# Performance work log

Hardware: AMD Instinct MI355X
Metric: run time of the kernel (lower is better)

## Reference

```python
import jax, jax.numpy as jnp
import numpy as np

BETA = 0.25  # commitment_beta


def setup_inputs() -> dict:
    key = jax.random.key(0)
    k1, k2 = jax.random.split(key)
    B, S, D, K = 4, 2048, 256, 8192
    z_e = jax.random.normal(k1, (B, S, D), dtype=jnp.float32)
    # codebook init ~ uniform(-1/K, 1/K) in the original; scale is irrelevant for correctness,
    # use normal scaled similarly small.
    codebook = jax.random.uniform(k2, (K, D), dtype=jnp.float32, minval=-1.0 / K, maxval=1.0 / K)
    return {"z_e": z_e, "codebook": codebook}


def reference(z_e, codebook):
    B, S, D = z_e.shape
    flat = z_e.reshape(-1, D)  # [N, D], N = B*S
    distances = (
        jnp.sum(flat * flat, axis=1, keepdims=True)
        - 2.0 * (flat @ codebook.T)
        + jnp.sum(codebook * codebook, axis=1)[None, :]
    )
    indices = jnp.argmin(distances, axis=1)  # [N]
    z_q = codebook[indices].reshape(B, S, D)
    codebook_loss = jnp.mean((jax.lax.stop_gradient(z_e) - z_q) ** 2)
    commitment_loss = jnp.mean((z_e - jax.lax.stop_gradient(z_q)) ** 2)
    vq_loss = codebook_loss + BETA * commitment_loss
    # straight-through estimator
    z_q_st = z_e + jax.lax.stop_gradient(z_q - z_e)
    return z_q_st, indices.reshape(B, S), vq_loss
```

## Files before the change

kernel.cpp:

```cpp
#include <hip/hip_runtime.h>
#include <stdint.h>

#define N_ROWS  8192
#define DIM     256
#define K_CODES 8192
#define SPLITK  8
#define KS      1024
#define ROWS_B  64
#define KT_CODES 256
#define LSLOTS  32
#define GSLOTS  8
#define MARGIN_ACC 1.0e-4f

typedef unsigned long long u64;
typedef unsigned short u16;
typedef short s16x8 __attribute__((ext_vector_type(8)));
typedef float f32x4 __attribute__((ext_vector_type(4)));

__device__ __forceinline__ u64 u64min(u64 a, u64 b) { return a < b ? a : b; }

__device__ __forceinline__ u16 f2bf(float f) {
    unsigned u = __float_as_uint(f);
    u += 0x7fffu + ((u >> 16) & 1u);
    return (u16)(u >> 16);
}

__device__ __forceinline__ unsigned fkey(float f) {
    unsigned b = __float_as_uint(f);
    return (b & 0x80000000u) ? ~b : (b | 0x80000000u);
}
__device__ __forceinline__ float funkey(unsigned k) {
    unsigned b = (k & 0x80000000u) ? (k ^ 0x80000000u) : ~k;
    return __uint_as_float(b);
}

__device__ __forceinline__ void gld16(void* lds, const void* g) {
    __builtin_amdgcn_global_load_lds(
        (const __attribute__((address_space(1))) unsigned int*)g,
        (__attribute__((address_space(3))) unsigned int*)lds, 16, 0, 0);
}

__device__ __forceinline__ float exact_dot(const float* __restrict__ xr,
                                           const float* __restrict__ cr) {
    const float4* x4 = (const float4*)xr;
    const float4* c4 = (const float4*)cr;
    float acc = 0.0f;
#pragma unroll 8
    for (int c = 0; c < DIM / 4; c++) {
        float4 xv = x4[c], cv = c4[c];
        acc = __builtin_fmaf(xv.x, cv.x, acc);
        acc = __builtin_fmaf(xv.y, cv.y, acc);
        acc = __builtin_fmaf(xv.z, cv.z, acc);
        acc = __builtin_fmaf(xv.w, cv.w, acc);
    }
    return acc;
}

__global__ __launch_bounds__(256) void vq_prep(const float* __restrict__ z_e,
                                               const float* __restrict__ cb,
                                               u16* __restrict__ zb,
                                               u16* __restrict__ cbb,
                                               float* __restrict__ xnorm,
                                               float* __restrict__ cnorm) {
    int wid  = (blockIdx.x * 256 + threadIdx.x) >> 6;
    int lane = threadIdx.x & 63;
    const float* src; u16* d16; float* dn;
    if (wid < N_ROWS) { src = z_e + (size_t)wid * DIM; d16 = zb + (size_t)wid * DIM; dn = xnorm + wid; }
    else              { int k = wid - N_ROWS;
                        src = cb  + (size_t)k   * DIM; d16 = cbb + (size_t)k * DIM; dn = cnorm + k; }
    float4 v = *(const float4*)(src + lane * 4);
    ushort4 h;
    h.x = f2bf(v.x); h.y = f2bf(v.y); h.z = f2bf(v.z); h.w = f2bf(v.w);
    *(ushort4*)(d16 + lane * 4) = h;
    float s = (v.x * v.x + v.y * v.y) + (v.z * v.z + v.w * v.w);
#pragma unroll
    for (int off = 1; off < 64; off <<= 1)
        s += __shfl_xor(s, off, 64);
    if (lane == 0) *dn = s;
}

__global__ __launch_bounds__(256, 3) void vq_mfma(const u16* __restrict__ zb,
                                                  const u16* __restrict__ cbb,
                                                  int* __restrict__ cand_cnt,
                                                  u64* __restrict__ candkey) {
    __shared__ u16      Xs[ROWS_B * DIM];
    __shared__ float    lcd[ROWS_B * LSLOTS];
    __shared__ int      lci[ROWS_B * LSLOTS];
    __shared__ int      lcnt[ROWS_B];
    __shared__ unsigned smax[ROWS_B];

    const int tid   = threadIdx.x;
    const int lane  = tid & 63;
    const int wave  = tid >> 6;
    const int quad  = lane >> 4;
    const int l16   = lane & 15;
    const int split = blockIdx.x;
    const int n0    = blockIdx.y * ROWS_B;

    if (tid < ROWS_B) { lcnt[tid] = 0; smax[tid] = 0u; }

#pragma unroll
    for (int t = 0; t < 8; t++) {
        int ubase = wave * 512 + t * 64;
        int u     = ubase + lane;
        int row   = u >> 5;
        int p     = u & 31;
        int csrc  = p ^ (row & 7);
        gld16(&Xs[ubase * 8], zb + (size_t)(n0 + row) * DIM + csrc * 8);
    }
    __syncthreads();

    for (int kt = 0; kt < KS / KT_CODES; kt++) {
        const int kw = split * KS + kt * KT_CODES + wave * 64;
        f32x4 acc[4][4];
#pragma unroll
        for (int i = 0; i < 4; i++)
#pragma unroll
            for (int j = 0; j < 4; j++)
#pragma unroll
                for (int e = 0; e < 4; e++) acc[i][j][e] = 0.0f;

#pragma unroll
        for (int ks = 0; ks < 8; ks++) {
            s16x8 af[4], bfr[4];
#pragma unroll
            for (int i = 0; i < 4; i++)
                af[i] = *(const s16x8*)&Xs[(i * 16 + l16) * DIM +
                                           (((ks << 2) | quad) ^ (l16 & 7)) * 8];
#pragma unroll
            for (int j = 0; j < 4; j++)
                bfr[j] = *(const s16x8*)(cbb + (size_t)(kw + j * 16 + l16) * DIM +
                                         ks * 32 + quad * 8);
#pragma unroll
            for (int i = 0; i < 4; i++)
#pragma unroll
                for (int j = 0; j < 4; j++)
                    acc[i][j] = __builtin_amdgcn_mfma_f32_16x16x32_bf16(af[i], bfr[j], acc[i][j], 0, 0, 0);
        }

#pragma unroll
        for (int i = 0; i < 4; i++)
#pragma unroll
            for (int r = 0; r < 4; r++) {
                int rl = i * 16 + quad * 4 + r;
                float m = fmaxf(fmaxf(acc[i][0][r], acc[i][1][r]),
                                fmaxf(acc[i][2][r], acc[i][3][r]));
                m = fmaxf(m, __shfl_xor(m, 1, 64));
                m = fmaxf(m, __shfl_xor(m, 2, 64));
                m = fmaxf(m, __shfl_xor(m, 4, 64));
                m = fmaxf(m, __shfl_xor(m, 8, 64));
                if (l16 == 0) atomicMax(&smax[rl], fkey(m));
                float g   = funkey(smax[rl]);
                float thr = fmaxf(g, m) - MARGIN_ACC;
                float mj = fmaxf(fmaxf(acc[i][0][r], acc[i][1][r]),
                                 fmaxf(acc[i][2][r], acc[i][3][r]));
                if (mj >= thr) {
#pragma unroll
                    for (int j = 0; j < 4; j++) {
                        float d = acc[i][j][r];
                        if (d >= thr) {
                            int pos = atomicAdd(&lcnt[rl], 1);
                            if (pos < LSLOTS) {
                                lcd[rl * LSLOTS + pos] = d;
                                lci[rl * LSLOTS + pos] = kw + j * 16 + l16;
                            }
                        }
                    }
                }
            }
    }

    __syncthreads();

    if (tid < ROWS_B) {
        int   row  = tid, n = n0 + row;
        int   raw  = lcnt[row];
        int   cnt  = raw < LSLOTS ? raw : LSLOTS;
        float thr  = funkey(smax[row]) - MARGIN_ACC;
        int   base = (n * SPLITK + split) * GSLOTS;
        int   w = 0, kept = 0;
        for (int s = 0; s < cnt; s++) {
            if (lcd[row * LSLOTS + s] >= thr) {
                kept++;
                if (w < GSLOTS) {
                    float d = lcd[row * LSLOTS + s];
                    candkey[base + w] = ((u64)__float_as_uint(d) << 32)
                                        | (unsigned)lci[row * LSLOTS + s];
                    w++;
                }
            }
        }
        cand_cnt[n * SPLITK + split] = (raw > LSLOTS || kept > GSLOTS) ? -1 : w;
    }
}

__global__ __launch_bounds__(256) void vq_finalize(const float* __restrict__ z_e,
                                                   const float* __restrict__ cb,
                                                   const float* __restrict__ xnorm,
                                                   const float* __restrict__ cnorm,
                                                   const int* __restrict__ cand_cnt,
                                                   const u64* __restrict__ candkey,
                                                   float* __restrict__ out_zq,
                                                   float* __restrict__ out_idx,
                                                   float* __restrict__ rowloss) {
    const int n    = blockIdx.x * 4 + (threadIdx.x >> 6);
    const int lane = threadIdx.x & 63;
    const int s    = lane >> 3;
    const int t    = lane & 7;

    const float* xr = z_e + (size_t)n * DIM;
    const float  xn = xnorm[n];

    int  cnt   = cand_cnt[n * SPLITK + s];
    u64  ck    = candkey[(size_t)n * 64 + lane];
    bool valid = (cnt >= 0) && (t < cnt);
    float dot  = valid ? __uint_as_float((unsigned)(ck >> 32)) : -3.0e38f;

    float gmax = dot;
#pragma unroll
    for (int off = 1; off < 64; off <<= 1)
        gmax = fmaxf(gmax, __shfl_xor(gmax, off, 64));
    float thr = gmax - MARGIN_ACC;

    u64 key = ~0ULL;
    if (valid && dot >= thr) {
        int  idx   = (int)(unsigned)(ck & 0xffffffffu);
        float m    = exact_dot(xr, cb + (size_t)idx * DIM);
        float dist = __builtin_fmaf(-2.0f, m, xn) + cnorm[idx];
        key = ((u64)__float_as_uint(dist) << 32) | (unsigned)idx;
    }

#pragma unroll
    for (int fs = 0; fs < SPLITK; fs++) {
        if (__builtin_expect(cand_cnt[n * SPLITK + fs] < 0, 0)) {
            for (int it = 0; it < KS / 64; it++) {
                int k = fs * KS + it * 64 + lane;
                float m    = exact_dot(xr, cb + (size_t)k * DIM);
                float dist = __builtin_fmaf(-2.0f, m, xn) + cnorm[k];
                key = u64min(key, ((u64)__float_as_uint(dist) << 32) | (unsigned)k);
            }
        }
    }

#pragma unroll
    for (int off = 1; off < 64; off <<= 1)
        key = u64min(key, __shfl_xor(key, off, 64));

    int idx = (int)(unsigned)(key & 0xffffffffu);
    if (key == ~0ULL) idx = 0;

    float4 x = *(const float4*)(xr + lane * 4);
    float4 c = *(const float4*)(cb + (size_t)idx * DIM + lane * 4);
    float4 st;
    st.x = x.x + (c.x - x.x); st.y = x.y + (c.y - x.y);
    st.z = x.z + (c.z - x.z); st.w = x.w + (c.w - x.w);
    *(float4*)(out_zq + (size_t)n * DIM + lane * 4) = st;

    float d0 = x.x - c.x, d1 = x.y - c.y, d2 = x.z - c.z, d3 = x.w - c.w;
    float s2 = (d0 * d0 + d1 * d1) + (d2 * d2 + d3 * d3);
#pragma unroll
    for (int off = 1; off < 64; off <<= 1)
        s2 += __shfl_xor(s2, off, 64);
    if (lane == 0) {
        rowloss[n] = s2;
        out_idx[n] = (float)idx;
    }
}

__global__ __launch_bounds__(256) void vq_loss(const float* __restrict__ rowloss,
                                               float* __restrict__ out_loss) {
    __shared__ double sd[256];
    double s = 0.0;
    for (int i = threadIdx.x; i < N_ROWS; i += 256) s += (double)rowloss[i];
    sd[threadIdx.x] = s;
    __syncthreads();
    for (int off = 128; off; off >>= 1) {
        if (threadIdx.x < off) sd[threadIdx.x] += sd[threadIdx.x + off];
        __syncthreads();
    }
    if (threadIdx.x == 0) {
        double mean = sd[0] / (double)((size_t)N_ROWS * DIM);
        out_loss[0] = (float)(1.25 * mean);
    }
}

extern "C" void kernel_launch(void* const* d_in, const int* in_sizes, int n_in,
                              void* d_out, int out_size, void* d_ws, size_t ws_size,
                              hipStream_t stream) {
    const float* z_e = (const float*)d_in[0];
    const float* cb  = (const float*)d_in[1];

    float* out   = (float*)d_out;
    float* zq    = out;
    float* oidx  = out + (size_t)N_ROWS * DIM;
    float* oloss = oidx + N_ROWS;

    u16*   zb       = (u16*)d_ws;
    u16*   cbb      = zb + (size_t)N_ROWS * DIM;
    float* xnorm    = (float*)(cbb + (size_t)K_CODES * DIM);
    float* cnorm    = xnorm + N_ROWS;
    float* rowloss  = cnorm + K_CODES;
    int*   cand_cnt = (int*)(rowloss + N_ROWS);
    u64*   candkey  = (u64*)(cand_cnt + N_ROWS * SPLITK);

    vq_prep    <<<(N_ROWS + K_CODES) / 4, 256, 0, stream>>>(z_e, cb, zb, cbb, xnorm, cnorm);
    vq_mfma    <<<dim3(SPLITK, N_ROWS / ROWS_B), 256, 0, stream>>>(zb, cbb, cand_cnt, candkey);
    vq_finalize<<<N_ROWS / 4, 256, 0, stream>>>(z_e, cb, xnorm, cnorm, cand_cnt, candkey, zq, oidx, rowloss);
    vq_loss    <<<1, 256, 0, stream>>>(rowloss, oloss);
}
```

Measured before the change: 200.9 us.

## Prefetch codebook fragments into registers and replace loss reduction with atomics

The MFMA kernel now loads all 32 B-fragments for a K-tile into registers before the MFMA loop, with a sched_barrier to keep the loads grouped ahead of compute. Launch bounds occupancy drops from 3 to 2 waves to make room for the extra registers. The row-loss buffer and its block-reduction kernel are replaced by a double atomicAdd per row in finalize, plus a tiny final kernel. The double accumulator is zeroed in prep. The trade-off is lower occupancy and atomic contention in exchange for more memory-level parallelism and less reduction work.

```diff
diff --git a/kernel.cpp b/kernel.cpp
--- a/kernel.cpp
+++ b/kernel.cpp
@@ -61,7 +61,9 @@
                                                u16* __restrict__ zb,
                                                u16* __restrict__ cbb,
                                                float* __restrict__ xnorm,
-                                               float* __restrict__ cnorm) {
+                                               float* __restrict__ cnorm,
+                                               double* __restrict__ dacc) {
+    if (blockIdx.x == 0 && threadIdx.x == 0) *dacc = 0.0;
     int wid  = (blockIdx.x * 256 + threadIdx.x) >> 6;
     int lane = threadIdx.x & 63;
     const float* src; u16* d16; float* dn;
@@ -79,7 +81,7 @@
     if (lane == 0) *dn = s;
 }
 
-__global__ __launch_bounds__(256, 3) void vq_mfma(const u16* __restrict__ zb,
+__global__ __launch_bounds__(256, 2) void vq_mfma(const u16* __restrict__ zb,
                                                   const u16* __restrict__ cbb,
                                                   int* __restrict__ cand_cnt,
                                                   u64* __restrict__ candkey) {
@@ -112,6 +114,16 @@
 
     for (int kt = 0; kt < KS / KT_CODES; kt++) {
         const int kw = split * KS + kt * KT_CODES + wave * 64;
+        const u16* bbase = cbb + (size_t)(kw + l16) * DIM + quad * 8;
+
+        s16x8 bb[32];
+#pragma unroll
+        for (int ks = 0; ks < 8; ks++)
+#pragma unroll
+            for (int j = 0; j < 4; j++)
+                bb[j * 8 + ks] = *(const s16x8*)(bbase + (size_t)(j * 16) * DIM + ks * 32);
+        __builtin_amdgcn_sched_barrier(0);
+
         f32x4 acc[4][4];
 #pragma unroll
         for (int i = 0; i < 4; i++)
@@ -122,20 +134,16 @@
 
 #pragma unroll
         for (int ks = 0; ks < 8; ks++) {
-            s16x8 af[4], bfr[4];
+            s16x8 af[4];
 #pragma unroll
             for (int i = 0; i < 4; i++)
                 af[i] = *(const s16x8*)&Xs[(i * 16 + l16) * DIM +
                                            (((ks << 2) | quad) ^ (l16 & 7)) * 8];
 #pragma unroll
-            for (int j = 0; j < 4; j++)
-                bfr[j] = *(const s16x8*)(cbb + (size_t)(kw + j * 16 + l16) * DIM +
-                                         ks * 32 + quad * 8);
-#pragma unroll
             for (int i = 0; i < 4; i++)
 #pragma unroll
                 for (int j = 0; j < 4; j++)
-                    acc[i][j] = __builtin_amdgcn_mfma_f32_16x16x32_bf16(af[i], bfr[j], acc[i][j], 0, 0, 0);
+                    acc[i][j] = __builtin_amdgcn_mfma_f32_16x16x32_bf16(af[i], bb[j * 8 + ks], acc[i][j], 0, 0, 0);
         }
 
 #pragma unroll
@@ -202,7 +210,7 @@
                                                    const u64* __restrict__ candkey,
                                                    float* __restrict__ out_zq,
                                                    float* __restrict__ out_idx,
-                                                   float* __restrict__ rowloss) {
+                                                   double* __restrict__ dacc) {
     const int n    = blockIdx.x * 4 + (threadIdx.x >> 6);
     const int lane = threadIdx.x & 63;
     const int s    = lane >> 3;
@@ -262,26 +270,15 @@
     for (int off = 1; off < 64; off <<= 1)
         s2 += __shfl_xor(s2, off, 64);
     if (lane == 0) {
-        rowloss[n] = s2;
         out_idx[n] = (float)idx;
-    }
-}
-
-__global__ __launch_bounds__(256) void vq_loss(const float* __restrict__ rowloss,
-                                               float* __restrict__ out_loss) {
-    __shared__ double sd[256];
-    double s = 0.0;
-    for (int i = threadIdx.x; i < N_ROWS; i += 256) s += (double)rowloss[i];
-    sd[threadIdx.x] = s;
-    __syncthreads();
-    for (int off = 128; off; off >>= 1) {
-        if (threadIdx.x < off) sd[threadIdx.x] += sd[threadIdx.x + off];
-        __syncthreads();
-    }
-    if (threadIdx.x == 0) {
-        double mean = sd[0] / (double)((size_t)N_ROWS * DIM);
-        out_loss[0] = (float)(1.25 * mean);
-    }
+        atomicAdd(dacc, (double)s2);
+    }
+}
+
+__global__ void vq_loss_final(const double* __restrict__ dacc,
+                              float* __restrict__ out_loss) {
+    if (threadIdx.x == 0)
+        out_loss[0] = (float)(1.25 * (*dacc) / (double)((size_t)N_ROWS * DIM));
 }
 
 extern "C" void kernel_launch(void* const* d_in, const int* in_sizes, int n_in,
@@ -295,16 +292,16 @@
     float* oidx  = out + (size_t)N_ROWS * DIM;
     float* oloss = oidx + N_ROWS;
 
-    u16*   zb       = (u16*)d_ws;
-    u16*   cbb      = zb + (size_t)N_ROWS * DIM;
-    float* xnorm    = (float*)(cbb + (size_t)K_CODES * DIM);
-    float* cnorm    = xnorm + N_ROWS;
-    float* rowloss  = cnorm + K_CODES;
-    int*   cand_cnt = (int*)(rowloss + N_ROWS);
-    u64*   candkey  = (u64*)(cand_cnt + N_ROWS * SPLITK);
-
-    vq_prep    <<<(N_ROWS + K_CODES) / 4, 256, 0, stream>>>(z_e, cb, zb, cbb, xnorm, cnorm);
-    vq_mfma    <<<dim3(SPLITK, N_ROWS / ROWS_B), 256, 0, stream>>>(zb, cbb, cand_cnt, candkey);
-    vq_finalize<<<N_ROWS / 4, 256, 0, stream>>>(z_e, cb, xnorm, cnorm, cand_cnt, candkey, zq, oidx, rowloss);
-    vq_loss    <<<1, 256, 0, stream>>>(rowloss, oloss);
-}
+    u16*    zb       = (u16*)d_ws;
+    u16*    cbb      = zb + (size_t)N_ROWS * DIM;
+    float*  xnorm    = (float*)(cbb + (size_t)K_CODES * DIM);
+    float*  cnorm    = xnorm + N_ROWS;
+    double* dacc     = (double*)(cnorm + K_CODES);
+    int*    cand_cnt = (int*)(dacc + 1);
+    u64*    candkey  = (u64*)(cand_cnt + N_ROWS * SPLITK);
+
+    vq_prep      <<<(N_ROWS + K_CODES) / 4, 256, 0, stream>>>(z_e, cb, zb, cbb, xnorm, cnorm, dacc);
+    vq_mfma      <<<dim3(SPLITK, N_ROWS / ROWS_B), 256, 0, stream>>>(zb, cbb, cand_cnt, candkey);
+    vq_finalize  <<<N_ROWS / 4, 256, 0, stream>>>(z_e, cb, xnorm, cnorm, cand_cnt, candkey, zq, oidx, dacc);
+    vq_loss_final<<<1, 64, 0, stream>>>(dacc, oloss);
+}
```

New measurement: 277.7 us. +38.2%, slower.

## Double split-K factor and split finalize into pick and apply kernels

Applied to the files above, without the earlier changes.

Raises the codebook split from 8 to 16 chunks of 512 codes, doubling the MFMA grid so more workgroups run in parallel. The finalize step now handles 128 candidate slots per row, two per lane, and is split into a pick kernel that writes the chosen index and a separate apply kernel that writes z_q, the index and the row loss. This adds an extra kernel launch, an extra index buffer round trip, more candidate traffic and more exact re-ranking dot products per row.

```diff
diff --git a/kernel.cpp b/kernel.cpp
--- a/kernel.cpp
+++ b/kernel.cpp
@@ -4,8 +4,8 @@
 #define N_ROWS  8192
 #define DIM     256
 #define K_CODES 8192
-#define SPLITK  8
-#define KS      1024
+#define SPLITK  16
+#define KS      512
 #define ROWS_B  64
 #define KT_CODES 256
 #define LSLOTS  32
@@ -194,43 +194,50 @@
     }
 }
 
-__global__ __launch_bounds__(256) void vq_finalize(const float* __restrict__ z_e,
-                                                   const float* __restrict__ cb,
-                                                   const float* __restrict__ xnorm,
-                                                   const float* __restrict__ cnorm,
-                                                   const int* __restrict__ cand_cnt,
-                                                   const u64* __restrict__ candkey,
-                                                   float* __restrict__ out_zq,
-                                                   float* __restrict__ out_idx,
-                                                   float* __restrict__ rowloss) {
+__global__ __launch_bounds__(256) void vq_pick(const float* __restrict__ z_e,
+                                               const float* __restrict__ cb,
+                                               const float* __restrict__ xnorm,
+                                               const float* __restrict__ cnorm,
+                                               const int* __restrict__ cand_cnt,
+                                               const u64* __restrict__ candkey,
+                                               int* __restrict__ idx_out) {
     const int n    = blockIdx.x * 4 + (threadIdx.x >> 6);
     const int lane = threadIdx.x & 63;
-    const int s    = lane >> 3;
-    const int t    = lane & 7;
 
     const float* xr = z_e + (size_t)n * DIM;
     const float  xn = xnorm[n];
 
-    int  cnt   = cand_cnt[n * SPLITK + s];
-    u64  ck    = candkey[(size_t)n * 64 + lane];
-    bool valid = (cnt >= 0) && (t < cnt);
-    float dot  = valid ? __uint_as_float((unsigned)(ck >> 32)) : -3.0e38f;
-
-    float gmax = dot;
+    u64  ck[2];
+    bool valid[2];
+    float dot[2];
+#pragma unroll
+    for (int h = 0; h < 2; h++) {
+        int slot = h * 64 + lane;
+        int s    = slot >> 3;
+        int t    = slot & 7;
+        int cnt  = cand_cnt[n * SPLITK + s];
+        ck[h]    = candkey[(size_t)n * (SPLITK * GSLOTS) + slot];
+        valid[h] = (cnt >= 0) && (t < cnt);
+        dot[h]   = valid[h] ? __uint_as_float((unsigned)(ck[h] >> 32)) : -3.0e38f;
+    }
+
+    float gmax = fmaxf(dot[0], dot[1]);
 #pragma unroll
     for (int off = 1; off < 64; off <<= 1)
         gmax = fmaxf(gmax, __shfl_xor(gmax, off, 64));
     float thr = gmax - MARGIN_ACC;
 
     u64 key = ~0ULL;
-    if (valid && dot >= thr) {
-        int  idx   = (int)(unsigned)(ck & 0xffffffffu);
-        float m    = exact_dot(xr, cb + (size_t)idx * DIM);
-        float dist = __builtin_fmaf(-2.0f, m, xn) + cnorm[idx];
-        key = ((u64)__float_as_uint(dist) << 32) | (unsigned)idx;
-    }
-
-#pragma unroll
+#pragma unroll
+    for (int h = 0; h < 2; h++) {
+        if (valid[h] && dot[h] >= thr) {
+            int  idx   = (int)(unsigned)(ck[h] & 0xffffffffu);
+            float m    = exact_dot(xr, cb + (size_t)idx * DIM);
+            float dist = __builtin_fmaf(-2.0f, m, xn) + cnorm[idx];
+            key = u64min(key, ((u64)__float_as_uint(dist) << 32) | (unsigned)idx);
+        }
+    }
+
     for (int fs = 0; fs < SPLITK; fs++) {
         if (__builtin_expect(cand_cnt[n * SPLITK + fs] < 0, 0)) {
             for (int it = 0; it < KS / 64; it++) {
@@ -246,10 +253,24 @@
     for (int off = 1; off < 64; off <<= 1)
         key = u64min(key, __shfl_xor(key, off, 64));
 
-    int idx = (int)(unsigned)(key & 0xffffffffu);
-    if (key == ~0ULL) idx = 0;
-
-    float4 x = *(const float4*)(xr + lane * 4);
+    if (lane == 0) {
+        int idx = (int)(unsigned)(key & 0xffffffffu);
+        if (key == ~0ULL) idx = 0;
+        idx_out[n] = idx;
+    }
+}
+
+__global__ __launch_bounds__(64) void vq_apply(const float* __restrict__ z_e,
+                                               const float* __restrict__ cb,
+                                               const int* __restrict__ idx_in,
+                                               float* __restrict__ out_zq,
+                                               float* __restrict__ out_idx,
+                                               float* __restrict__ rowloss) {
+    int n    = blockIdx.x;
+    int lane = threadIdx.x;
+    int idx  = idx_in[n];
+
+    float4 x = *(const float4*)(z_e + (size_t)n * DIM + lane * 4);
     float4 c = *(const float4*)(cb + (size_t)idx * DIM + lane * 4);
     float4 st;
     st.x = x.x + (c.x - x.x); st.y = x.y + (c.y - x.y);
@@ -300,11 +321,13 @@
     float* xnorm    = (float*)(cbb + (size_t)K_CODES * DIM);
     float* cnorm    = xnorm + N_ROWS;
     float* rowloss  = cnorm + K_CODES;
-    int*   cand_cnt = (int*)(rowloss + N_ROWS);
+    int*   idxw     = (int*)(rowloss + N_ROWS);
+    int*   cand_cnt = idxw + N_ROWS;
     u64*   candkey  = (u64*)(cand_cnt + N_ROWS * SPLITK);
 
-    vq_prep    <<<(N_ROWS + K_CODES) / 4, 256, 0, stream>>>(z_e, cb, zb, cbb, xnorm, cnorm);
-    vq_mfma    <<<dim3(SPLITK, N_ROWS / ROWS_B), 256, 0, stream>>>(zb, cbb, cand_cnt, candkey);
-    vq_finalize<<<N_ROWS / 4, 256, 0, stream>>>(z_e, cb, xnorm, cnorm, cand_cnt, candkey, zq, oidx, rowloss);
-    vq_loss    <<<1, 256, 0, stream>>>(rowloss, oloss);
-}
+    vq_prep <<<(N_ROWS + K_CODES) / 4, 256, 0, stream>>>(z_e, cb, zb, cbb, xnorm, cnorm);
+    vq_mfma <<<dim3(SPLITK, N_ROWS / ROWS_B), 256, 0, stream>>>(zb, cbb, cand_cnt, candkey);
+    vq_pick <<<N_ROWS / 4, 256, 0, stream>>>(z_e, cb, xnorm, cnorm, cand_cnt, candkey, idxw);
+    vq_apply<<<N_ROWS, 64, 0, stream>>>(z_e, cb, idxw, zq, oidx, rowloss);
+    vq_loss <<<1, 256, 0, stream>>>(rowloss, oloss);
+}
```

Measured after the change: 234.3 us. +16.6%, slower.

## Double split-K, shrink candidate slots, and restage exact rescoring through LDS

Applied to the files above, without the earlier changes.

Splits the codebook search across 16 slices of 512 codes instead of 8 of 1024, lowers per-row local candidate slots, and raises the occupancy hint of the MFMA kernel to 4 blocks. The finalize kernel becomes one 64-thread block per row that gathers threshold-passing candidates into shared memory and rescores them in fp32 from LDS-staged codebook rows, instead of each lane doing a strided global dot product. The loss reduction now uses a 1024-thread block. The aim is more parallelism in the search and cheaper candidate rescoring, at the cost of twice as many candidate entries to merge and a higher chance of slot overflow falling back to brute-force slices.

```diff
diff --git a/kernel.cpp b/kernel.cpp
--- a/kernel.cpp
+++ b/kernel.cpp
@@ -4,12 +4,13 @@
 #define N_ROWS  8192
 #define DIM     256
 #define K_CODES 8192
-#define SPLITK  8
-#define KS      1024
+#define SPLITK  16
+#define KS      512
 #define ROWS_B  64
 #define KT_CODES 256
-#define LSLOTS  32
+#define LSLOTS  12
 #define GSLOTS  8
+#define MAXS    16
 #define MARGIN_ACC 1.0e-4f
 
 typedef unsigned long long u64;
@@ -40,8 +41,8 @@
         (__attribute__((address_space(3))) unsigned int*)lds, 16, 0, 0);
 }
 
-__device__ __forceinline__ float exact_dot(const float* __restrict__ xr,
-                                           const float* __restrict__ cr) {
+__device__ __forceinline__ float exact_dot_g(const float* __restrict__ xr,
+                                             const float* __restrict__ cr) {
     const float4* x4 = (const float4*)xr;
     const float4* c4 = (const float4*)cr;
     float acc = 0.0f;
@@ -79,7 +80,7 @@
     if (lane == 0) *dn = s;
 }
 
-__global__ __launch_bounds__(256, 3) void vq_mfma(const u16* __restrict__ zb,
+__global__ __launch_bounds__(256, 4) void vq_mfma(const u16* __restrict__ zb,
                                                   const u16* __restrict__ cbb,
                                                   int* __restrict__ cand_cnt,
                                                   u64* __restrict__ candkey) {
@@ -194,48 +195,96 @@
     }
 }
 
-__global__ __launch_bounds__(256) void vq_finalize(const float* __restrict__ z_e,
-                                                   const float* __restrict__ cb,
-                                                   const float* __restrict__ xnorm,
-                                                   const float* __restrict__ cnorm,
-                                                   const int* __restrict__ cand_cnt,
-                                                   const u64* __restrict__ candkey,
-                                                   float* __restrict__ out_zq,
-                                                   float* __restrict__ out_idx,
-                                                   float* __restrict__ rowloss) {
-    const int n    = blockIdx.x * 4 + (threadIdx.x >> 6);
-    const int lane = threadIdx.x & 63;
-    const int s    = lane >> 3;
-    const int t    = lane & 7;
+__global__ __launch_bounds__(64) void vq_pick_apply(const float* __restrict__ z_e,
+                                                    const float* __restrict__ cb,
+                                                    const float* __restrict__ xnorm,
+                                                    const float* __restrict__ cnorm,
+                                                    const int* __restrict__ cand_cnt,
+                                                    const u64* __restrict__ candkey,
+                                                    float* __restrict__ out_zq,
+                                                    float* __restrict__ out_idx,
+                                                    float* __restrict__ rowloss) {
+    __shared__ float xs[DIM];
+    __shared__ float cs[4][DIM + 4];
+    __shared__ int   sidx[MAXS];
+    __shared__ int   scnt;
+
+    const int n    = blockIdx.x;
+    const int lane = threadIdx.x;
+    if (lane == 0) scnt = 0;
 
     const float* xr = z_e + (size_t)n * DIM;
     const float  xn = xnorm[n];
-
-    int  cnt   = cand_cnt[n * SPLITK + s];
-    u64  ck    = candkey[(size_t)n * 64 + lane];
-    bool valid = (cnt >= 0) && (t < cnt);
-    float dot  = valid ? __uint_as_float((unsigned)(ck >> 32)) : -3.0e38f;
-
-    float gmax = dot;
+    float4 x = *(const float4*)(xr + lane * 4);
+    *(float4*)&xs[lane * 4] = x;
+
+    u64  ck0 = candkey[(size_t)n * (SPLITK * GSLOTS) + lane];
+    u64  ck1 = candkey[(size_t)n * (SPLITK * GSLOTS) + 64 + lane];
+    int  c0  = cand_cnt[n * SPLITK + (lane >> 3)];
+    int  c1  = cand_cnt[n * SPLITK + 8 + (lane >> 3)];
+    bool v0  = (c0 >= 0) && ((lane & 7) < c0);
+    bool v1  = (c1 >= 0) && ((lane & 7) < c1);
+    float d0 = v0 ? __uint_as_float((unsigned)(ck0 >> 32)) : -3.0e38f;
+    float d1 = v1 ? __uint_as_float((unsigned)(ck1 >> 32)) : -3.0e38f;
+
+    float gmax = fmaxf(d0, d1);
 #pragma unroll
     for (int off = 1; off < 64; off <<= 1)
         gmax = fmaxf(gmax, __shfl_xor(gmax, off, 64));
     float thr = gmax - MARGIN_ACC;
 
     u64 key = ~0ULL;
-    if (valid && dot >= thr) {
-        int  idx   = (int)(unsigned)(ck & 0xffffffffu);
-        float m    = exact_dot(xr, cb + (size_t)idx * DIM);
-        float dist = __builtin_fmaf(-2.0f, m, xn) + cnorm[idx];
-        key = ((u64)__float_as_uint(dist) << 32) | (unsigned)idx;
-    }
-
-#pragma unroll
+    if (v0 && d0 >= thr) {
+        int p = atomicAdd(&scnt, 1);
+        int idx = (int)(unsigned)(ck0 & 0xffffffffu);
+        if (p < MAXS) sidx[p] = idx;
+        else {
+            float m = exact_dot_g(xr, cb + (size_t)idx * DIM);
+            float dist = __builtin_fmaf(-2.0f, m, xn) + cnorm[idx];
+            key = u64min(key, ((u64)__float_as_uint(dist) << 32) | (unsigned)idx);
+        }
+    }
+    if (v1 && d1 >= thr) {
+        int p = atomicAdd(&scnt, 1);
+        int idx = (int)(unsigned)(ck1 & 0xffffffffu);
+        if (p < MAXS) sidx[p] = idx;
+        else {
+            float m = exact_dot_g(xr, cb + (size_t)idx * DIM);
+            float dist = __builtin_fmaf(-2.0f, m, xn) + cnorm[idx];
+            key = u64min(key, ((u64)__float_as_uint(dist) << 32) | (unsigned)idx);
+        }
+    }
+    __syncthreads();
+
+    int sc = scnt; if (sc > MAXS) sc = MAXS;
+    for (int b = 0; b < sc; b += 4) {
+        int take = sc - b; if (take > 4) take = 4;
+        int g   = lane >> 4;
+        int l16 = lane & 15;
+        if (g < take) {
+            const float* cr = cb + (size_t)sidx[b + g] * DIM;
+#pragma unroll
+            for (int p = 0; p < 4; p++)
+                *(float4*)&cs[g][p * 64 + l16 * 4] = *(const float4*)(cr + p * 64 + l16 * 4);
+        }
+        __syncthreads();
+        if (lane < take) {
+            int idx = sidx[b + lane];
+            float acc = 0.0f;
+#pragma unroll 8
+            for (int d = 0; d < DIM; d++)
+                acc = __builtin_fmaf(xs[d], cs[lane][d], acc);
+            float dist = __builtin_fmaf(-2.0f, acc, xn) + cnorm[idx];
+            key = u64min(key, ((u64)__float_as_uint(dist) << 32) | (unsigned)idx);
+        }
+        __syncthreads();
+    }
+
     for (int fs = 0; fs < SPLITK; fs++) {
         if (__builtin_expect(cand_cnt[n * SPLITK + fs] < 0, 0)) {
             for (int it = 0; it < KS / 64; it++) {
                 int k = fs * KS + it * 64 + lane;
-                float m    = exact_dot(xr, cb + (size_t)k * DIM);
+                float m    = exact_dot_g(xr, cb + (size_t)k * DIM);
                 float dist = __builtin_fmaf(-2.0f, m, xn) + cnorm[k];
                 key = u64min(key, ((u64)__float_as_uint(dist) << 32) | (unsigned)k);
             }
@@ -249,15 +298,14 @@
     int idx = (int)(unsigned)(key & 0xffffffffu);
     if (key == ~0ULL) idx = 0;
 
-    float4 x = *(const float4*)(xr + lane * 4);
     float4 c = *(const float4*)(cb + (size_t)idx * DIM + lane * 4);
     float4 st;
     st.x = x.x + (c.x - x.x); st.y = x.y + (c.y - x.y);
     st.z = x.z + (c.z - x.z); st.w = x.w + (c.w - x.w);
     *(float4*)(out_zq + (size_t)n * DIM + lane * 4) = st;
 
-    float d0 = x.x - c.x, d1 = x.y - c.y, d2 = x.z - c.z, d3 = x.w - c.w;
-    float s2 = (d0 * d0 + d1 * d1) + (d2 * d2 + d3 * d3);
+    float e0 = x.x - c.x, e1 = x.y - c.y, e2 = x.z - c.z, e3 = x.w - c.w;
+    float s2 = (e0 * e0 + e1 * e1) + (e2 * e2 + e3 * e3);
 #pragma unroll
     for (int off = 1; off < 64; off <<= 1)
         s2 += __shfl_xor(s2, off, 64);
@@ -267,14 +315,14 @@
     }
 }
 
-__global__ __launch_bounds__(256) void vq_loss(const float* __restrict__ rowloss,
-                                               float* __restrict__ out_loss) {
-    __shared__ double sd[256];
+__global__ __launch_bounds__(1024) void vq_loss(const float* __restrict__ rowloss,
+                                                float* __restrict__ out_loss) {
+    __shared__ double sd[1024];
     double s = 0.0;
-    for (int i = threadIdx.x; i < N_ROWS; i += 256) s += (double)rowloss[i];
+    for (int i = threadIdx.x; i < N_ROWS; i += 1024) s += (double)rowloss[i];
     sd[threadIdx.x] = s;
     __syncthreads();
-    for (int off = 128; off; off >>= 1) {
+    for (int off = 512; off; off >>= 1) {
         if (threadIdx.x < off) sd[threadIdx.x] += sd[threadIdx.x + off];
         __syncthreads();
     }
@@ -303,8 +351,8 @@
     int*   cand_cnt = (int*)(rowloss + N_ROWS);
     u64*   candkey  = (u64*)(cand_cnt + N_ROWS * SPLITK);
 
-    vq_prep    <<<(N_ROWS + K_CODES) / 4, 256, 0, stream>>>(z_e, cb, zb, cbb, xnorm, cnorm);
-    vq_mfma    <<<dim3(SPLITK, N_ROWS / ROWS_B), 256, 0, stream>>>(zb, cbb, cand_cnt, candkey);
-    vq_finalize<<<N_ROWS / 4, 256, 0, stream>>>(z_e, cb, xnorm, cnorm, cand_cnt, candkey, zq, oidx, rowloss);
-    vq_loss    <<<1, 256, 0, stream>>>(rowloss, oloss);
-}
+    vq_prep      <<<(N_ROWS + K_CODES) / 4, 256, 0, stream>>>(z_e, cb, zb, cbb, xnorm, cnorm);
+    vq_mfma      <<<dim3(SPLITK, N_ROWS / ROWS_B), 256, 0, stream>>>(zb, cbb, cand_cnt, candkey);
+    vq_pick_apply<<<N_ROWS, 64, 0, stream>>>(z_e, cb, xnorm, cnorm, cand_cnt, candkey, zq, oidx, rowloss);
+    vq_loss      <<<1, 1024, 0, stream>>>(rowloss, oloss);
+}
```

After: 230.8 us. 1.15x slower.
